# Performance work log

Hardware: AMD Instinct MI355X
Metric: run time of the kernel (lower is better)

The kernel has to match this reference:

```python
import jax, jax.numpy as jnp
import numpy as np

B, C, L = 8, 512, 2048   # batch, input_dim (channels), sequence length
H = 8                    # multihead_cnt
K = 3                    # kernel_dim
DH = C // H              # per-head dim = 64
SCALE = 1.0 / float(np.sqrt(C))  # module divides by sqrt(input_dim), not sqrt(head_dim)


def _conv1d(x, w, b):
    # x: [B, C, L], w: [C_out, C_in, K], padding=1 keeps L
    y = jax.lax.conv_general_dilated(x, w, window_strides=(1,), padding=[(1, 1)],
                                     dimension_numbers=('NCH', 'OIH', 'NCH'))
    return y + b[None, :, None]


def setup_inputs() -> dict:
    key = jax.random.key(0)
    ks = jax.random.split(key, 7)
    x = jax.random.normal(ks[0], (B, C, L), dtype=jnp.float32)
    # xavier_normal_ std for Conv1d weight [C, C, K]: sqrt(2 / (fan_in + fan_out)), fan = C*K
    std = float(np.sqrt(2.0 / (C * K + C * K)))
    inp = {'x': x}
    for i in range(3):  # conv_cnt = 3 -> q, k, v convolutions
        inp[f'w{i}'] = jax.random.normal(ks[1 + 2 * i], (C, C, K), dtype=jnp.float32) * std
        inp[f'b{i}'] = jax.random.normal(ks[2 + 2 * i], (C,), dtype=jnp.float32) * 0.01
    return inp


def reference(x, w0, b0, w1, b1, w2, b2):
    # q, k, v projections via Conv1d (padding preserves length)
    q = _conv1d(x, w0, b0)  # [B, C, L]
    k = _conv1d(x, w1, b1)
    v = _conv1d(x, w2, b2)
    # torch.chunk along dim 1 == contiguous reshape into heads
    qh = q.reshape(B, H, DH, L)
    kh = k.reshape(B, H, DH, L)
    vh = v.reshape(B, H, DH, L)
    # scores = q^T k / sqrt(input_dim)  -> [B, H, L, L]
    scores = jnp.einsum('bhdl,bhdm->bhlm', qh, kh) * SCALE
    att = jax.nn.softmax(scores, axis=-1)
    # out = (att @ v^T)^T -> [B, H, DH, L]
    out = jnp.einsum('bhlm,bhdm->bhdl', att, vh)
    return out.reshape(B, C, L)
```

## Files before the change

### kernel.cpp

```cpp
#include <hip/hip_runtime.h>
#include <hip/hip_bf16.h>
#include <cstdint>

typedef unsigned short u16;
typedef short v8s __attribute__((ext_vector_type(8)));
typedef float v4f __attribute__((ext_vector_type(4)));
typedef u16 u16x8 __attribute__((ext_vector_type(8)));
typedef u16 u16x4 __attribute__((ext_vector_type(4)));

static constexpr int Bb = 8, Cc = 512, Ll = 2048, Hh = 8, Dh = 64;

__device__ __forceinline__ float bf2f(u16 u){
  unsigned x = ((unsigned)u) << 16; float f; __builtin_memcpy(&f, &x, 4); return f;
}
__device__ __forceinline__ u16 f2bf(float f){
  unsigned x; __builtin_memcpy(&x, &f, 4);
  x = (x + 0x7fffu + ((x >> 16) & 1u)) >> 16; return (u16)x;
}

__device__ __forceinline__ void async_cp16(const u16* g, u16* l){
  __builtin_amdgcn_global_load_lds(
      (const __attribute__((address_space(1))) unsigned int*)g,
      (__attribute__((address_space(3))) unsigned int*)l, 16, 0, 0);
}

#if __has_builtin(__builtin_amdgcn_exp2f)
#define EXP2F(x) __builtin_amdgcn_exp2f(x)
#else
#define EXP2F(x) exp2f(x)
#endif

__global__ __launch_bounds__(256) void detect_dtype(const u16* __restrict__ x, unsigned* __restrict__ flag){
  __shared__ int cnt;
  if (threadIdx.x == 0) cnt = 0;
  __syncthreads();
  int sane = 0;
  for (int i = threadIdx.x; i < 4096; i += 256){
    unsigned e = (x[2 * i] >> 7) & 0xFFu;
    sane += (e >= 90u && e <= 160u) ? 1 : 0;
  }
  atomicAdd(&cnt, sane);
  __syncthreads();
  if (threadIdx.x == 0) *flag = (cnt < 2458) ? 1u : 0u;
}

__global__ __launch_bounds__(256) void transpose_pad(const void* __restrict__ xv, const unsigned* __restrict__ flagp,
                                                     u16* __restrict__ xT){
  int b = blockIdx.z, ci0 = blockIdx.y * 64, l0 = blockIdx.x * 64;
  __shared__ u16 tb[64 * 72];
  const unsigned isf32 = *flagp;
  int t = threadIdx.x;
  int row = t >> 3, seg = t & 7;
  if (isf32){
    const float* xf = (const float*)xv;
    #pragma unroll
    for (int rnd = 0; rnd < 2; rnd++){
      int ci = row + rnd * 32;
      size_t off = ((size_t)(b * Cc + ci0 + ci)) * Ll + l0 + seg * 8;
      v4f a = *(const v4f*)(xf + off);
      v4f c4 = *(const v4f*)(xf + off + 4);
      #pragma unroll
      for (int j = 0; j < 4; j++) tb[(seg * 8 + j) * 72 + ci] = f2bf(a[j]);
      #pragma unroll
      for (int j = 0; j < 4; j++) tb[(seg * 8 + 4 + j) * 72 + ci] = f2bf(c4[j]);
    }
  } else {
    const u16* x = (const u16*)xv;
    #pragma unroll
    for (int rnd = 0; rnd < 2; rnd++){
      int ci = row + rnd * 32;
      u16x8 v = *(const u16x8*)(x + ((size_t)(b * Cc + ci0 + ci)) * Ll + l0 + seg * 8);
      #pragma unroll
      for (int j = 0; j < 8; j++) tb[(seg * 8 + j) * 72 + ci] = v[j];
    }
  }
  __syncthreads();
  #pragma unroll
  for (int rnd = 0; rnd < 2; rnd++){
    int l = row + rnd * 32;
    u16x8 v = *(const u16x8*)&tb[l * 72 + seg * 8];
    *(u16x8*)(xT + ((size_t)b * 2050 + 1 + l0 + l) * Cc + ci0 + seg * 8) = v;
  }
  if (blockIdx.x == 0 && t < 8){
    u16x8 z = {};
    *(u16x8*)(xT + ((size_t)b * 2050 + 0) * Cc + ci0 + t * 8) = z;
  }
  if (blockIdx.x == 31 && t < 8){
    u16x8 z = {};
    *(u16x8*)(xT + ((size_t)b * 2050 + 2049) * Cc + ci0 + t * 8) = z;
  }
}

__global__ __launch_bounds__(256) void pack_wb(const void* __restrict__ w0, const void* __restrict__ w1,
                                               const void* __restrict__ w2, const void* __restrict__ b0,
                                               const void* __restrict__ b1, const void* __restrict__ b2,
                                               const unsigned* __restrict__ flagp,
                                               u16* __restrict__ wp, u16* __restrict__ bb){
  int g = blockIdx.x * 256 + threadIdx.x;
  const unsigned isf32 = *flagp;
  if (g < 9 * 512 * 512){
    int ci = g & 511, co = (g >> 9) & 511, kc = g >> 18;
    int conv = kc / 3, k = kc - conv * 3;
    const void* w = (conv == 0) ? w0 : ((conv == 1) ? w1 : w2);
    size_t idx = (size_t)co * 1536 + ci * 3 + k;
    wp[g] = isf32 ? f2bf(((const float*)w)[idx]) : ((const u16*)w)[idx];
  } else {
    int g2 = g - 9 * 512 * 512;
    if (g2 < 1536){
      int conv = g2 >> 9, c = g2 & 511;
      const void* bsrc = (conv == 0) ? b0 : ((conv == 1) ? b1 : b2);
      bb[g2] = isf32 ? f2bf(((const float*)bsrc)[c]) : ((const u16*)bsrc)[c];
    }
  }
}

__global__ __launch_bounds__(256) void conv_gemm_fused(const u16* __restrict__ wp, const u16* __restrict__ xT,
                                                       const u16* __restrict__ bb, u16* __restrict__ qT,
                                                       u16* __restrict__ kT, u16* __restrict__ vN){
  int b = blockIdx.y, bx = blockIdx.x;
  int mt = bx >> 3, nt = bx & 7;
  int m0 = mt * 128, n0 = nt * 256;
  int conv = m0 >> 9;
  int co0 = m0 & 511;
  __shared__ u16 smem[12288 + 8256];
  u16* lA = smem;
  u16* lB = smem + 12288;
  int t = threadIdx.x, wave = t >> 6, lane = t & 63, quad = lane >> 4, lid = lane & 15;
  int wm = (wave >> 1) * 64, wn = (wave & 1) * 128;
  v4f acc[4][8] = {};
  const size_t xbase = (size_t)b * 2050 * Cc;

  for (int it = 0; it < 16; it++){
    int ci0 = it << 5;
    #pragma unroll
    for (int r = 0; r < 4; r++){
      int e = (r * 256 + t) * 8;
      int row = e >> 5, cio = e & 31;
      async_cp16(xT + xbase + (size_t)(n0 + row) * 512 + ci0 + cio, &lB[e]);
    }
    #pragma unroll
    for (int r = 0; r < 6; r++){
      int e = (r * 256 + t) * 8;
      int ks = e >> 12, rem = e & 4095, row = rem >> 5, cio = rem & 31;
      async_cp16(wp + ((size_t)((conv * 3 + ks) * 512 + co0 + row)) * 512 + ci0 + cio, &lA[e]);
    }
    if (t < 8){
      int hr = 256 + (t >> 2), cio = (t & 3) * 8;
      u16x8 hv = *(const u16x8*)(xT + xbase + (size_t)(n0 + hr) * 512 + ci0 + cio);
      *(u16x8*)&lB[hr * 32 + cio] = hv;
    }
    __syncthreads();
    #pragma unroll
    for (int ks = 0; ks < 3; ks++){
      v8s aF[4], bF[8];
      #pragma unroll
      for (int i = 0; i < 4; i++) aF[i] = *(const v8s*)&lA[ks * 4096 + (wm + i * 16 + lid) * 32 + quad * 8];
      #pragma unroll
      for (int j = 0; j < 8; j++) bF[j] = *(const v8s*)&lB[(wn + j * 16 + lid + ks) * 32 + quad * 8];
      #pragma unroll
      for (int i = 0; i < 4; i++)
        #pragma unroll
        for (int j = 0; j < 8; j++)
          acc[i][j] = __builtin_amdgcn_mfma_f32_16x16x32_bf16(aF[i], bF[j], acc[i][j], 0, 0, 0);
    }
    __syncthreads();
  }

  const float qsc = (float)(1.4426950408889634 / 22.627416997969522);
  if (conv < 2){
    u16* dst = (conv == 0) ? qT : kT;
    #pragma unroll
    for (int i = 0; i < 4; i++){
      int cog = m0 + wm + i * 16 + quad * 4;
      float bv[4];
      #pragma unroll
      for (int r = 0; r < 4; r++) bv[r] = bf2f(bb[cog + r]);
      int co = cog & 511;
      #pragma unroll
      for (int j = 0; j < 8; j++){
        int l = n0 + wn + j * 16 + lid;
        u16x4 pk;
        #pragma unroll
        for (int r = 0; r < 4; r++){
          float v = acc[i][j][r] + bv[r];
          if (conv == 0) v *= qsc;
          pk[r] = f2bf(v);
        }
        *(u16x4*)(dst + ((((size_t)b * Hh + (co >> 6)) * Ll + l) << 6) + (co & 63)) = pk;
      }
    }
  } else {
    u16* scr = smem;
    #pragma unroll
    for (int cs = 0; cs < 2; cs++){
      __syncthreads();
      #pragma unroll
      for (int i = 0; i < 4; i++){
        int cog = m0 + wm + i * 16 + quad * 4;
        float bv[4];
        #pragma unroll
        for (int r = 0; r < 4; r++) bv[r] = bf2f(bb[cog + r]);
        #pragma unroll
        for (int j = 0; j < 4; j++){
          int jj = cs * 4 + j;
          int lcl = (wave & 1) * 64 + j * 16 + lid;
          #pragma unroll
          for (int r = 0; r < 4; r++)
            scr[(wm + i * 16 + quad * 4 + r) * 130 + lcl] = f2bf(acc[i][jj][r] + bv[r]);
        }
      }
      __syncthreads();
      int row = t & 127, half = t >> 7;
      int co = co0 + row;
      size_t gb = (((size_t)b * Cc + co) << 11) + n0 + half * 128 + cs * 64;
      #pragma unroll
      for (int s = 0; s < 8; s++){
        u16x8 vv = *(const u16x8*)&scr[row * 130 + half * 64 + s * 8];
        *(u16x8*)(vN + gb + s * 8) = vv;
      }
    }
  }
}

__global__ __launch_bounds__(256) void attn_kernel(const u16* __restrict__ qT, const u16* __restrict__ kT,
                                                   const u16* __restrict__ vN, const unsigned* __restrict__ flagp,
                                                   void* __restrict__ outv){
  int bhx = blockIdx.x;
  int b = bhx >> 3, h = bhx & 7, l0 = blockIdx.y * 128;
  int t = threadIdx.x, w = t >> 6, lane = t & 63, quad = lane >> 4, lid = lane & 15;
  __shared__ u16 kls[128 * 72];
  __shared__ u16 vls[64 * 136];
  const unsigned isf32 = *flagp;
  const size_t bh = (size_t)b * Hh + h;

  int kadd[5], vadd[5];
  bool kval[5], vval[5];
  #pragma unroll
  for (int r = 0; r < 5; r++){
    int e = (r * 256 + t) * 8;
    kval[r] = e < 128 * 72;
    int slot = e / 72, off = e - slot * 72;
    int s5 = slot & 31;
    int m = (slot & ~31) | (((s5 >> 2) & 1) << 3) | (((s5 >> 3) & 1) << 4) | (((s5 >> 4) & 1) << 2) | (s5 & 3);
    kadd[r] = m * 64 + (off < 64 ? off : 0);
    vval[r] = e < 64 * 136;
    int d = e / 136, voff = e - d * 136;
    vadd[r] = d * Ll + (voff < 128 ? voff : 0);
  }
  const u16* kTb = kT + bh * Ll * 64;
  const u16* vNb = vN + ((size_t)(b * Cc + h * Dh)) * Ll;

  v8s qF[2][2];
  #pragma unroll
  for (int ci = 0; ci < 2; ci++)
    #pragma unroll
    for (int ks = 0; ks < 2; ks++)
      qF[ci][ks] = *(const v8s*)(qT + ((bh * Ll) + l0 + w * 32 + ci * 16 + lid) * 64 + ks * 32 + quad * 8);

  const v8s onesF = {0x3F80, 0x3F80, 0x3F80, 0x3F80, 0x3F80, 0x3F80, 0x3F80, 0x3F80};
  v4f o[2][4] = {};
  v4f o1[2] = {};

  for (int mt = 0; mt < 16; mt++){
    int m0 = mt * 128;
    const u16* kt = kTb + (size_t)m0 * 64;
    const u16* vt = vNb + m0;
    #pragma unroll
    for (int r = 0; r < 5; r++)
      if (kval[r]) async_cp16(kt + kadd[r], &kls[(r * 256 + t) * 8]);
    #pragma unroll
    for (int r = 0; r < 5; r++)
      if (vval[r]) async_cp16(vt + vadd[r], &vls[(r * 256 + t) * 8]);
    __syncthreads();

    v4f s[4][2][2] = {};
    #pragma unroll
    for (int ks = 0; ks < 2; ks++){
      v8s aF[4][2];
      #pragma unroll
      for (int c = 0; c < 4; c++)
        #pragma unroll
        for (int tt = 0; tt < 2; tt++)
          aF[c][tt] = *(const v8s*)&kls[(c * 32 + tt * 16 + lid) * 72 + ks * 32 + quad * 8];
      #pragma unroll
      for (int c = 0; c < 4; c++)
        #pragma unroll
        for (int tt = 0; tt < 2; tt++){
          s[c][tt][0] = __builtin_amdgcn_mfma_f32_16x16x32_bf16(aF[c][tt], qF[0][ks], s[c][tt][0], 0, 0, 0);
          s[c][tt][1] = __builtin_amdgcn_mfma_f32_16x16x32_bf16(aF[c][tt], qF[1][ks], s[c][tt][1], 0, 0, 0);
        }
    }

    #pragma unroll
    for (int c = 0; c < 4; c++){
      v8s aP[2];
      #pragma unroll
      for (int ci = 0; ci < 2; ci++){
        float p[8];
        #pragma unroll
        for (int tt = 0; tt < 2; tt++)
          #pragma unroll
          for (int r = 0; r < 4; r++)
            p[tt * 4 + r] = EXP2F(s[c][tt][ci][r]);
        unsigned u[4];
        #pragma unroll
        for (int k2 = 0; k2 < 4; k2++){
          __hip_bfloat162 hb = __float22bfloat162_rn(make_float2(p[2 * k2], p[2 * k2 + 1]));
          __builtin_memcpy(&u[k2], &hb, 4);
        }
        __builtin_memcpy(&aP[ci], u, 16);
      }
      v8s bV[4];
      #pragma unroll
      for (int df = 0; df < 4; df++)
        bV[df] = *(const v8s*)&vls[(df * 16 + lid) * 136 + c * 32 + quad * 8];
      #pragma unroll
      for (int ci = 0; ci < 2; ci++){
        #pragma unroll
        for (int df = 0; df < 4; df++)
          o[ci][df] = __builtin_amdgcn_mfma_f32_16x16x32_bf16(aP[ci], bV[df], o[ci][df], 0, 0, 0);
        o1[ci] = __builtin_amdgcn_mfma_f32_16x16x32_bf16(aP[ci], onesF, o1[ci], 0, 0, 0);
      }
    }
    __syncthreads();
  }

  #pragma unroll
  for (int lf = 0; lf < 2; lf++){
    v4f nv;
    #pragma unroll
    for (int r = 0; r < 4; r++) nv[r] = 1.f / o1[lf][r];
    #pragma unroll
    for (int df = 0; df < 4; df++){
      int d = df * 16 + lid;
      int l = l0 + w * 32 + lf * 16 + quad * 4;
      size_t ofs = (((bh << 6) + d) << 11) + l;
      if (isf32){
        v4f st;
        #pragma unroll
        for (int r = 0; r < 4; r++) st[r] = o[lf][df][r] * nv[r];
        *(v4f*)((float*)outv + ofs) = st;
      } else {
        u16x4 pk;
        #pragma unroll
        for (int r = 0; r < 4; r++) pk[r] = f2bf(o[lf][df][r] * nv[r]);
        *(u16x4*)((u16*)outv + ofs) = pk;
      }
    }
  }
}

extern "C" void kernel_launch(void* const* d_in, const int* in_sizes, int n_in,
                              void* d_out, int out_size, void* d_ws, size_t ws_size,
                              hipStream_t stream){
  const void* x  = d_in[0];
  const void* w0 = d_in[1];
  const void* b0 = d_in[2];
  const void* w1 = d_in[3];
  const void* b1 = d_in[4];
  const void* w2 = d_in[5];
  const void* b2 = d_in[6];
  u16* ws = (u16*)d_ws;
  unsigned* flag = (unsigned*)ws;
  u16* xT = ws + 64;
  u16* wp = xT + (size_t)8 * 2050 * 512;
  u16* bb = wp + (size_t)9 * 512 * 512;
  u16* qT = bb + 1536;
  u16* kT = qT + (size_t)8 * 8 * 2048 * 64;
  u16* vN = kT + (size_t)8 * 8 * 2048 * 64;

  detect_dtype<<<1, 256, 0, stream>>>((const u16*)x, flag);
  transpose_pad<<<dim3(32, 8, 8), 256, 0, stream>>>(x, flag, xT);
  pack_wb<<<dim3(9 * 512 * 512 / 256 + 6), 256, 0, stream>>>(w0, w1, w2, b0, b1, b2, flag, wp, bb);
  conv_gemm_fused<<<dim3(96, 8), 256, 0, stream>>>(wp, xT, bb, qT, kT, vN);
  attn_kernel<<<dim3(64, 16), 256, 0, stream>>>(qT, kT, vN, flag, d_out);
}
```

Baseline: 297.5 us.

## Double-buffer K/V in attention, enlarge query tile, merge prep kernels

The attention kernel now double-buffers the K/V shared-memory tiles, issuing async loads for the next tile while computing on the current one. Each block now covers 256 query rows (64 per wave) instead of 128, which halves the grid and reuses each K/V tile across more queries. The score computation is reorganised per 32-key chunk to limit live registers. Separately, the input transpose and weight/bias packing are merged into one prep kernel, with vectorised weight reorder loads, and the conv scratch row stride is changed from 130 to 136. The trade-off is higher register and LDS use per block and fewer blocks on the device, which can lower occupancy.

```diff
diff --git a/kernel.cpp b/kernel.cpp
--- a/kernel.cpp
+++ b/kernel.cpp
@@ -44,68 +44,88 @@
   if (threadIdx.x == 0) *flag = (cnt < 2458) ? 1u : 0u;
 }
 
-__global__ __launch_bounds__(256) void transpose_pad(const void* __restrict__ xv, const unsigned* __restrict__ flagp,
-                                                     u16* __restrict__ xT){
-  int b = blockIdx.z, ci0 = blockIdx.y * 64, l0 = blockIdx.x * 64;
+__global__ __launch_bounds__(256) void prep_kernel(const void* __restrict__ xv,
+                                                   const void* __restrict__ w0, const void* __restrict__ w1,
+                                                   const void* __restrict__ w2, const void* __restrict__ b0,
+                                                   const void* __restrict__ b1, const void* __restrict__ b2,
+                                                   const unsigned* __restrict__ flagp,
+                                                   u16* __restrict__ xT, u16* __restrict__ wp,
+                                                   u16* __restrict__ bb){
   __shared__ u16 tb[64 * 72];
   const unsigned isf32 = *flagp;
-  int t = threadIdx.x;
-  int row = t >> 3, seg = t & 7;
-  if (isf32){
-    const float* xf = (const float*)xv;
+  int blk = blockIdx.x, t = threadIdx.x;
+  if (blk < 2048){
+    int b = blk >> 8, ci0 = ((blk >> 5) & 7) * 64, l0 = (blk & 31) * 64;
+    int row = t >> 3, seg = t & 7;
+    if (isf32){
+      const float* xf = (const float*)xv;
+      #pragma unroll
+      for (int rnd = 0; rnd < 2; rnd++){
+        int ci = row + rnd * 32;
+        size_t off = ((size_t)(b * Cc + ci0 + ci)) * Ll + l0 + seg * 8;
+        v4f a = *(const v4f*)(xf + off);
+        v4f c4 = *(const v4f*)(xf + off + 4);
+        #pragma unroll
+        for (int j = 0; j < 4; j++) tb[(seg * 8 + j) * 72 + ci] = f2bf(a[j]);
+        #pragma unroll
+        for (int j = 0; j < 4; j++) tb[(seg * 8 + 4 + j) * 72 + ci] = f2bf(c4[j]);
+      }
+    } else {
+      const u16* x = (const u16*)xv;
+      #pragma unroll
+      for (int rnd = 0; rnd < 2; rnd++){
+        int ci = row + rnd * 32;
+        u16x8 v = *(const u16x8*)(x + ((size_t)(b * Cc + ci0 + ci)) * Ll + l0 + seg * 8);
+        #pragma unroll
+        for (int j = 0; j < 8; j++) tb[(seg * 8 + j) * 72 + ci] = v[j];
+      }
+    }
+    __syncthreads();
     #pragma unroll
     for (int rnd = 0; rnd < 2; rnd++){
-      int ci = row + rnd * 32;
-      size_t off = ((size_t)(b * Cc + ci0 + ci)) * Ll + l0 + seg * 8;
-      v4f a = *(const v4f*)(xf + off);
-      v4f c4 = *(const v4f*)(xf + off + 4);
-      #pragma unroll
-      for (int j = 0; j < 4; j++) tb[(seg * 8 + j) * 72 + ci] = f2bf(a[j]);
-      #pragma unroll
-      for (int j = 0; j < 4; j++) tb[(seg * 8 + 4 + j) * 72 + ci] = f2bf(c4[j]);
+      int l = row + rnd * 32;
+      u16x8 v = *(const u16x8*)&tb[l * 72 + seg * 8];
+      *(u16x8*)(xT + ((size_t)b * 2050 + 1 + l0 + l) * Cc + ci0 + seg * 8) = v;
+    }
+    if ((blk & 31) == 0 && t < 8){
+      u16x8 z = {};
+      *(u16x8*)(xT + ((size_t)b * 2050 + 0) * Cc + ci0 + t * 8) = z;
+    }
+    if ((blk & 31) == 31 && t < 8){
+      u16x8 z = {};
+      *(u16x8*)(xT + ((size_t)b * 2050 + 2049) * Cc + ci0 + t * 8) = z;
+    }
+  } else if (blk < 2432){
+    int g = (blk - 2048) * 256 + t;
+    int conv = g >> 15, rem = g & 32767, co = rem >> 6, cig = rem & 63;
+    const void* w = (conv == 0) ? w0 : ((conv == 1) ? w1 : w2);
+    u16 in24[24];
+    if (isf32){
+      const float* wf = (const float*)w + (size_t)co * 1536 + cig * 24;
+      #pragma unroll
+      for (int v = 0; v < 6; v++){
+        v4f t4 = *(const v4f*)(wf + v * 4);
+        #pragma unroll
+        for (int r = 0; r < 4; r++) in24[v * 4 + r] = f2bf(t4[r]);
+      }
+    } else {
+      const u16* wu = (const u16*)w + (size_t)co * 1536 + cig * 24;
+      #pragma unroll
+      for (int v = 0; v < 3; v++){
+        u16x8 t8 = *(const u16x8*)(wu + v * 8);
+        #pragma unroll
+        for (int r = 0; r < 8; r++) in24[v * 8 + r] = t8[r];
+      }
+    }
+    #pragma unroll
+    for (int k = 0; k < 3; k++){
+      u16x8 ov;
+      #pragma unroll
+      for (int i = 0; i < 8; i++) ov[i] = in24[i * 3 + k];
+      *(u16x8*)(wp + ((size_t)((conv * 3 + k) * 512 + co)) * 512 + cig * 8) = ov;
     }
   } else {
-    const u16* x = (const u16*)xv;
-    #pragma unroll
-    for (int rnd = 0; rnd < 2; rnd++){
-      int ci = row + rnd * 32;
-      u16x8 v = *(const u16x8*)(x + ((size_t)(b * Cc + ci0 + ci)) * Ll + l0 + seg * 8);
-      #pragma unroll
-      for (int j = 0; j < 8; j++) tb[(seg * 8 + j) * 72 + ci] = v[j];
-    }
-  }
-  __syncthreads();
-  #pragma unroll
-  for (int rnd = 0; rnd < 2; rnd++){
-    int l = row + rnd * 32;
-    u16x8 v = *(const u16x8*)&tb[l * 72 + seg * 8];
-    *(u16x8*)(xT + ((size_t)b * 2050 + 1 + l0 + l) * Cc + ci0 + seg * 8) = v;
-  }
-  if (blockIdx.x == 0 && t < 8){
-    u16x8 z = {};
-    *(u16x8*)(xT + ((size_t)b * 2050 + 0) * Cc + ci0 + t * 8) = z;
-  }
-  if (blockIdx.x == 31 && t < 8){
-    u16x8 z = {};
-    *(u16x8*)(xT + ((size_t)b * 2050 + 2049) * Cc + ci0 + t * 8) = z;
-  }
-}
-
-__global__ __launch_bounds__(256) void pack_wb(const void* __restrict__ w0, const void* __restrict__ w1,
-                                               const void* __restrict__ w2, const void* __restrict__ b0,
-                                               const void* __restrict__ b1, const void* __restrict__ b2,
-                                               const unsigned* __restrict__ flagp,
-                                               u16* __restrict__ wp, u16* __restrict__ bb){
-  int g = blockIdx.x * 256 + threadIdx.x;
-  const unsigned isf32 = *flagp;
-  if (g < 9 * 512 * 512){
-    int ci = g & 511, co = (g >> 9) & 511, kc = g >> 18;
-    int conv = kc / 3, k = kc - conv * 3;
-    const void* w = (conv == 0) ? w0 : ((conv == 1) ? w1 : w2);
-    size_t idx = (size_t)co * 1536 + ci * 3 + k;
-    wp[g] = isf32 ? f2bf(((const float*)w)[idx]) : ((const u16*)w)[idx];
-  } else {
-    int g2 = g - 9 * 512 * 512;
+    int g2 = (blk - 2432) * 256 + t;
     if (g2 < 1536){
       int conv = g2 >> 9, c = g2 & 511;
       const void* bsrc = (conv == 0) ? b0 : ((conv == 1) ? b1 : b2);
@@ -123,8 +143,6 @@
   int conv = m0 >> 9;
   int co0 = m0 & 511;
   __shared__ u16 smem[12288 + 8256];
-  u16* lA = smem;
-  u16* lB = smem + 12288;
   int t = threadIdx.x, wave = t >> 6, lane = t & 63, quad = lane >> 4, lid = lane & 15;
   int wm = (wave >> 1) * 64, wn = (wave & 1) * 128;
   v4f acc[4][8] = {};
@@ -132,17 +150,19 @@
 
   for (int it = 0; it < 16; it++){
     int ci0 = it << 5;
+    u16* lA = smem;
+    u16* lB = smem + 12288;
     #pragma unroll
     for (int r = 0; r < 4; r++){
       int e = (r * 256 + t) * 8;
       int row = e >> 5, cio = e & 31;
-      async_cp16(xT + xbase + (size_t)(n0 + row) * 512 + ci0 + cio, &lB[e]);
+      async_cp16(xT + xbase + (size_t)(n0 + row) * 512 + ci0 + cio, lB + e);
     }
     #pragma unroll
     for (int r = 0; r < 6; r++){
       int e = (r * 256 + t) * 8;
       int ks = e >> 12, rem = e & 4095, row = rem >> 5, cio = rem & 31;
-      async_cp16(wp + ((size_t)((conv * 3 + ks) * 512 + co0 + row)) * 512 + ci0 + cio, &lA[e]);
+      async_cp16(wp + ((size_t)((conv * 3 + ks) * 512 + co0 + row)) * 512 + ci0 + cio, lA + e);
     }
     if (t < 8){
       int hr = 256 + (t >> 2), cio = (t & 3) * 8;
@@ -206,7 +226,7 @@
           int lcl = (wave & 1) * 64 + j * 16 + lid;
           #pragma unroll
           for (int r = 0; r < 4; r++)
-            scr[(wm + i * 16 + quad * 4 + r) * 130 + lcl] = f2bf(acc[i][jj][r] + bv[r]);
+            scr[(wm + i * 16 + quad * 4 + r) * 136 + lcl] = f2bf(acc[i][jj][r] + bv[r]);
         }
       }
       __syncthreads();
@@ -215,7 +235,7 @@
       size_t gb = (((size_t)b * Cc + co) << 11) + n0 + half * 128 + cs * 64;
       #pragma unroll
       for (int s = 0; s < 8; s++){
-        u16x8 vv = *(const u16x8*)&scr[row * 130 + half * 64 + s * 8];
+        u16x8 vv = *(const u16x8*)&scr[row * 136 + half * 64 + s * 8];
         *(u16x8*)(vN + gb + s * 8) = vv;
       }
     }
@@ -226,10 +246,10 @@
                                                    const u16* __restrict__ vN, const unsigned* __restrict__ flagp,
                                                    void* __restrict__ outv){
   int bhx = blockIdx.x;
-  int b = bhx >> 3, h = bhx & 7, l0 = blockIdx.y * 128;
+  int b = bhx >> 3, h = bhx & 7, l0 = blockIdx.y * 256;
   int t = threadIdx.x, w = t >> 6, lane = t & 63, quad = lane >> 4, lid = lane & 15;
-  __shared__ u16 kls[128 * 72];
-  __shared__ u16 vls[64 * 136];
+  __shared__ u16 kls[2 * 128 * 72];
+  __shared__ u16 vls[2 * 64 * 136];
   const unsigned isf32 = *flagp;
   const size_t bh = (size_t)b * Hh + h;
 
@@ -250,58 +270,62 @@
   const u16* kTb = kT + bh * Ll * 64;
   const u16* vNb = vN + ((size_t)(b * Cc + h * Dh)) * Ll;
 
-  v8s qF[2][2];
+  auto stageKV = [&](int mt){
+    const u16* kt = kTb + (size_t)mt * 128 * 64;
+    const u16* vt = vNb + mt * 128;
+    u16* kdst = kls + (mt & 1) * (128 * 72);
+    u16* vdst = vls + (mt & 1) * (64 * 136);
+    #pragma unroll
+    for (int r = 0; r < 5; r++)
+      if (kval[r]) async_cp16(kt + kadd[r], &kdst[(r * 256 + t) * 8]);
+    #pragma unroll
+    for (int r = 0; r < 5; r++)
+      if (vval[r]) async_cp16(vt + vadd[r], &vdst[(r * 256 + t) * 8]);
+  };
+
+  stageKV(0);
+
+  v8s qF[4][2];
   #pragma unroll
-  for (int ci = 0; ci < 2; ci++)
+  for (int ci = 0; ci < 4; ci++)
     #pragma unroll
     for (int ks = 0; ks < 2; ks++)
-      qF[ci][ks] = *(const v8s*)(qT + ((bh * Ll) + l0 + w * 32 + ci * 16 + lid) * 64 + ks * 32 + quad * 8);
+      qF[ci][ks] = *(const v8s*)(qT + ((bh * Ll) + l0 + w * 64 + ci * 16 + lid) * 64 + ks * 32 + quad * 8);
 
   const v8s onesF = {0x3F80, 0x3F80, 0x3F80, 0x3F80, 0x3F80, 0x3F80, 0x3F80, 0x3F80};
-  v4f o[2][4] = {};
-  v4f o1[2] = {};
+  v4f o[4][4] = {};
+  v4f o1[4] = {};
+  __syncthreads();
 
   for (int mt = 0; mt < 16; mt++){
-    int m0 = mt * 128;
-    const u16* kt = kTb + (size_t)m0 * 64;
-    const u16* vt = vNb + m0;
-    #pragma unroll
-    for (int r = 0; r < 5; r++)
-      if (kval[r]) async_cp16(kt + kadd[r], &kls[(r * 256 + t) * 8]);
-    #pragma unroll
-    for (int r = 0; r < 5; r++)
-      if (vval[r]) async_cp16(vt + vadd[r], &vls[(r * 256 + t) * 8]);
-    __syncthreads();
-
-    v4f s[4][2][2] = {};
-    #pragma unroll
-    for (int ks = 0; ks < 2; ks++){
-      v8s aF[4][2];
-      #pragma unroll
-      for (int c = 0; c < 4; c++)
+    const u16* kcur = kls + (mt & 1) * (128 * 72);
+    const u16* vcur = vls + (mt & 1) * (64 * 136);
+    if (mt + 1 < 16) stageKV(mt + 1);
+
+    #pragma unroll
+    for (int c = 0; c < 4; c++){
+      v4f s[2][4] = {};
+      #pragma unroll
+      for (int ks = 0; ks < 2; ks++){
+        v8s aF[2];
         #pragma unroll
         for (int tt = 0; tt < 2; tt++)
-          aF[c][tt] = *(const v8s*)&kls[(c * 32 + tt * 16 + lid) * 72 + ks * 32 + quad * 8];
-      #pragma unroll
-      for (int c = 0; c < 4; c++)
-        #pragma unroll
-        for (int tt = 0; tt < 2; tt++){
-          s[c][tt][0] = __builtin_amdgcn_mfma_f32_16x16x32_bf16(aF[c][tt], qF[0][ks], s[c][tt][0], 0, 0, 0);
-          s[c][tt][1] = __builtin_amdgcn_mfma_f32_16x16x32_bf16(aF[c][tt], qF[1][ks], s[c][tt][1], 0, 0, 0);
-        }
-    }
-
-    #pragma unroll
-    for (int c = 0; c < 4; c++){
-      v8s aP[2];
-      #pragma unroll
-      for (int ci = 0; ci < 2; ci++){
+          aF[tt] = *(const v8s*)&kcur[(c * 32 + tt * 16 + lid) * 72 + ks * 32 + quad * 8];
+        #pragma unroll
+        for (int tt = 0; tt < 2; tt++)
+          #pragma unroll
+          for (int ci = 0; ci < 4; ci++)
+            s[tt][ci] = __builtin_amdgcn_mfma_f32_16x16x32_bf16(aF[tt], qF[ci][ks], s[tt][ci], 0, 0, 0);
+      }
+      v8s aP[4];
+      #pragma unroll
+      for (int ci = 0; ci < 4; ci++){
         float p[8];
         #pragma unroll
         for (int tt = 0; tt < 2; tt++)
           #pragma unroll
           for (int r = 0; r < 4; r++)
-            p[tt * 4 + r] = EXP2F(s[c][tt][ci][r]);
+            p[tt * 4 + r] = EXP2F(s[tt][ci][r]);
         unsigned u[4];
         #pragma unroll
         for (int k2 = 0; k2 < 4; k2++){
@@ -313,9 +337,9 @@
       v8s bV[4];
       #pragma unroll
       for (int df = 0; df < 4; df++)
-        bV[df] = *(const v8s*)&vls[(df * 16 + lid) * 136 + c * 32 + quad * 8];
-      #pragma unroll
-      for (int ci = 0; ci < 2; ci++){
+        bV[df] = *(const v8s*)&vcur[(df * 16 + lid) * 136 + c * 32 + quad * 8];
+      #pragma unroll
+      for (int ci = 0; ci < 4; ci++){
         #pragma unroll
         for (int df = 0; df < 4; df++)
           o[ci][df] = __builtin_amdgcn_mfma_f32_16x16x32_bf16(aP[ci], bV[df], o[ci][df], 0, 0, 0);
@@ -326,24 +350,24 @@
   }
 
   #pragma unroll
-  for (int lf = 0; lf < 2; lf++){
+  for (int ci = 0; ci < 4; ci++){
     v4f nv;
     #pragma unroll
-    for (int r = 0; r < 4; r++) nv[r] = 1.f / o1[lf][r];
+    for (int r = 0; r < 4; r++) nv[r] = 1.f / o1[ci][r];
     #pragma unroll
     for (int df = 0; df < 4; df++){
       int d = df * 16 + lid;
-      int l = l0 + w * 32 + lf * 16 + quad * 4;
+      int l = l0 + w * 64 + ci * 16 + quad * 4;
       size_t ofs = (((bh << 6) + d) << 11) + l;
       if (isf32){
         v4f st;
         #pragma unroll
-        for (int r = 0; r < 4; r++) st[r] = o[lf][df][r] * nv[r];
+        for (int r = 0; r < 4; r++) st[r] = o[ci][df][r] * nv[r];
         *(v4f*)((float*)outv + ofs) = st;
       } else {
         u16x4 pk;
         #pragma unroll
-        for (int r = 0; r < 4; r++) pk[r] = f2bf(o[lf][df][r] * nv[r]);
+        for (int r = 0; r < 4; r++) pk[r] = f2bf(o[ci][df][r] * nv[r]);
         *(u16x4*)((u16*)outv + ofs) = pk;
       }
     }
@@ -370,8 +394,7 @@
   u16* vN = kT + (size_t)8 * 8 * 2048 * 64;
 
   detect_dtype<<<1, 256, 0, stream>>>((const u16*)x, flag);
-  transpose_pad<<<dim3(32, 8, 8), 256, 0, stream>>>(x, flag, xT);
-  pack_wb<<<dim3(9 * 512 * 512 / 256 + 6), 256, 0, stream>>>(w0, w1, w2, b0, b1, b2, flag, wp, bb);
+  prep_kernel<<<dim3(2438), 256, 0, stream>>>(x, w0, w1, w2, b0, b1, b2, flag, xT, wp, bb);
   conv_gemm_fused<<<dim3(96, 8), 256, 0, stream>>>(wp, xT, bb, qT, kT, vN);
-  attn_kernel<<<dim3(64, 16), 256, 0, stream>>>(qT, kT, vN, flag, d_out);
-}
+  attn_kernel<<<dim3(64, 8), 256, 0, stream>>>(qT, kT, vN, flag, d_out);
+}
```

New measurement: 304.6 us. +2.4%, slower.
